# Kernel optimization log

Measured on AMD Instinct MI355X. Metric: run time of the kernel, lower is better.

The kernel has to match this reference:

```python
import jax, jax.numpy as jnp
import numpy as np

N_NODES = 10000
N_EDGES = 320000
IN_DIM, HID_DIM, OUT_DIM = 256, 512, 256


def gcn_conv(x, src, dst, W, b, n_nodes):
    """PyG GCNConv: add self-loops, symmetric deg normalization, linear, scatter-add, bias."""
    loops = jnp.arange(n_nodes, dtype=src.dtype)
    s = jnp.concatenate([src, loops])
    d = jnp.concatenate([dst, loops])
    deg = jax.ops.segment_sum(jnp.ones_like(s, dtype=x.dtype), d, num_segments=n_nodes)
    dinv = jax.lax.rsqrt(deg)  # deg >= 1 due to self-loops
    norm = dinv[s] * dinv[d]  # [E+N]
    h = x @ W  # [N, out]
    msg = h[s] * norm[:, None]  # [E+N, out]
    return jax.ops.segment_sum(msg, d, num_segments=n_nodes) + b


def setup_inputs() -> dict:
    key = jax.random.key(0)
    ks = jax.random.split(key, 8)
    x = jax.random.normal(ks[0], (N_NODES, IN_DIM), dtype=jnp.float32)
    edge_index = jax.random.randint(ks[1], (2, N_EDGES), 0, N_NODES, dtype=jnp.int64 if jax.config.jax_enable_x64 else jnp.int32)
    perturb_first = jax.random.normal(ks[2], (N_NODES, HID_DIM), dtype=jnp.float32)
    perturb_last = jax.random.normal(ks[3], (N_NODES, OUT_DIM), dtype=jnp.float32)
    W1 = jax.random.normal(ks[4], (IN_DIM, HID_DIM), dtype=jnp.float32) * (1.0 / np.sqrt(IN_DIM))
    b1 = jnp.zeros((HID_DIM,), dtype=jnp.float32)
    W2 = jax.random.normal(ks[5], (HID_DIM, OUT_DIM), dtype=jnp.float32) * (1.0 / np.sqrt(HID_DIM))
    b2 = jnp.zeros((OUT_DIM,), dtype=jnp.float32)
    return {"x": x, "edge_index": edge_index, "perturb_first": perturb_first,
            "perturb_last": perturb_last, "W1": W1, "b1": b1, "W2": W2, "b2": b2}


def reference(x, edge_index, perturb_first, perturb_last, W1, b1, W2, b2):
    # Faithful to Encoder_Adversarial_GCN.forward: only model[0] (conv1) and
    # model[3] (conv2) are applied; LayerNorm/PReLU layers are skipped.
    src, dst = edge_index[0], edge_index[1]
    h = gcn_conv(x, src, dst, W1, b1, N_NODES) + perturb_first
    out = gcn_conv(h, src, dst, W2, b2, N_NODES) + perturb_last
    return out
```

## Files before the change

### kernel.cpp

```cpp
#include <hip/hip_runtime.h>
#include <hip/hip_bf16.h>

#define NN 10000
#define NE 320000
#define IN_DIM 256
#define HID_DIM 512
#define OUT_DIM 256
#define CAP 96

typedef __attribute__((ext_vector_type(8))) short sh8;
typedef __attribute__((ext_vector_type(4))) float f32x4;

__device__ __forceinline__ ushort f2b(float f) {
    uint u = __builtin_bit_cast(uint, f);
    u = (u + 0x7FFFu + ((u >> 16) & 1u)) >> 16;
    return (ushort)u;
}
__device__ __forceinline__ float b2f(ushort h) {
    uint u = ((uint)h) << 16;
    return __builtin_bit_cast(float, u);
}

__device__ __forceinline__ void g2l16(const ushort* g, ushort* l) {
    __builtin_amdgcn_global_load_lds(
        (const __attribute__((address_space(1))) void*)g,
        (__attribute__((address_space(3))) void*)l,
        16, 0, 0);
}

__global__ void k_conv(const float* __restrict__ x, ushort* __restrict__ xb,
                       const float* __restrict__ W1, ushort* __restrict__ W1t,
                       const float* __restrict__ W2, ushort* __restrict__ W2t,
                       int* __restrict__ cursor) {
    const int b = blockIdx.x, t = threadIdx.x;
    if (b < 2500) {
        size_t i = ((size_t)b * 256 + t) * 4;
        float4 f = *(const float4*)&x[i];
        *(ushort4*)&xb[i] = make_ushort4(f2b(f.x), f2b(f.y), f2b(f.z), f2b(f.w));
    } else if (b < 3012) {
        int idx = (b - 2500) * 256 + t;
        int n = idx >> 8, k = idx & 255;
        W1t[idx] = f2b(W1[(size_t)k * HID_DIM + n]);
    } else if (b < 3524) {
        int idx = (b - 3012) * 256 + t;
        int n = idx >> 9, k = idx & 511;
        W2t[idx] = f2b(W2[(size_t)k * OUT_DIM + n]);
    } else {
        int idx = (b - 3524) * 256 + t;
        cursor[idx] = 0;
    }
}

__global__ void k_fill(const int* __restrict__ src, const int* __restrict__ dst,
                       int* cursor, int* __restrict__ edges, int e) {
    int i = blockIdx.x * blockDim.x + threadIdx.x;
    if (i < e) {
        int d = dst[i];
        int pos = atomicAdd(&cursor[d], 1);
        if (pos < CAP) edges[(size_t)d * CAP + pos] = src[i];
    }
}

template <bool FINAL>
__global__ __launch_bounds__(256) void k_agg(const ushort* __restrict__ tbl,
                                             const int* __restrict__ cnt,
                                             const int* __restrict__ edges,
                                             const float* __restrict__ bias,
                                             const float* __restrict__ pert,
                                             void* __restrict__ outv) {
    const int t = threadIdx.x;
    const int b = blockIdx.x;
    const int g = b & 7;
    const int dimhalf = g >> 2;
    const int nodeblk = (b >> 3) * 4 + (g & 3);
    const int v = nodeblk * 4 + (t >> 6);
    const int lane = t & 63;
    const int qtr = lane >> 4;
    const int d0 = dimhalf * 128 + (lane & 15) * 8;
    const int deg = min(cnt[v], CAP);
    const float dv = rsqrtf((float)(deg + 1));
    const int base = (deg * qtr) >> 2;
    const int n = ((deg * (qtr + 1)) >> 2) - base;
    const int* ep = edges + (size_t)v * CAP + base;

    float a[8];
    if (qtr == 0) {
        sh8 hv = *(const sh8*)&tbl[(size_t)v * 256 + d0];
#pragma unroll
        for (int j = 0; j < 8; ++j) a[j] = b2f((ushort)hv[j]) * dv;
    } else {
#pragma unroll
        for (int j = 0; j < 8; ++j) a[j] = 0.f;
    }

    int i = 0;
    for (; i + 2 <= n; i += 2) {
        int s0 = ep[i], s1 = ep[i + 1];
        float w0 = rsqrtf((float)(cnt[s0] + 1));
        float w1 = rsqrtf((float)(cnt[s1] + 1));
        sh8 r0 = *(const sh8*)&tbl[(size_t)s0 * 256 + d0];
        sh8 r1 = *(const sh8*)&tbl[(size_t)s1 * 256 + d0];
#pragma unroll
        for (int j = 0; j < 8; ++j) a[j] = fmaf(b2f((ushort)r0[j]), w0, a[j]);
#pragma unroll
        for (int j = 0; j < 8; ++j) a[j] = fmaf(b2f((ushort)r1[j]), w1, a[j]);
    }
    if (i < n) {
        int s0 = ep[i];
        float w0 = rsqrtf((float)(cnt[s0] + 1));
        sh8 r0 = *(const sh8*)&tbl[(size_t)s0 * 256 + d0];
#pragma unroll
        for (int j = 0; j < 8; ++j) a[j] = fmaf(b2f((ushort)r0[j]), w0, a[j]);
    }

#pragma unroll
    for (int j = 0; j < 8; ++j) {
        a[j] += __shfl_xor(a[j], 16);
        a[j] += __shfl_xor(a[j], 32);
        a[j] *= dv;
    }

    if (qtr == 0) {
        const size_t o = (size_t)v * 256 + d0;
        if (FINAL) {
            float* out = (float*)outv;
            float4 p0 = *(const float4*)&pert[o];
            float4 p1 = *(const float4*)&pert[o + 4];
            float4 b0 = *(const float4*)&bias[d0];
            float4 b1 = *(const float4*)&bias[d0 + 4];
            *(float4*)&out[o]     = make_float4(a[0] + b0.x + p0.x, a[1] + b0.y + p0.y,
                                                a[2] + b0.z + p0.z, a[3] + b0.w + p0.w);
            *(float4*)&out[o + 4] = make_float4(a[4] + b1.x + p1.x, a[5] + b1.y + p1.y,
                                                a[6] + b1.z + p1.z, a[7] + b1.w + p1.w);
        } else {
            ushort* out = (ushort*)outv;
            *(ushort4*)&out[o]     = make_ushort4(f2b(a[0]), f2b(a[1]), f2b(a[2]), f2b(a[3]));
            *(ushort4*)&out[o + 4] = make_ushort4(f2b(a[4]), f2b(a[5]), f2b(a[6]), f2b(a[7]));
        }
    }
}

template <bool BIAS>
__global__ __launch_bounds__(256) void k_gemm(const ushort* __restrict__ A,
                                              const ushort* __restrict__ Bt,
                                              const float* __restrict__ bias,
                                              const float* __restrict__ pert,
                                              ushort* __restrict__ C,
                                              int M, int N, int K) {
    __shared__ ushort As[64][64];
    __shared__ ushort Bs[64][64];
    const int T = gridDim.x;
    const int q = T >> 3, r = T & 7;
    const int xcd = blockIdx.x & 7, jj = blockIdx.x >> 3;
    const int tid = (xcd < r ? xcd * (q + 1) : r * (q + 1) + (xcd - r) * q) + jj;
    const int nbx = N >> 6;
    const int bm = (tid / nbx) * 64;
    const int bn = (tid % nbx) * 64;

    const int t = threadIdx.x;
    const int lane = t & 63;
    const int w = t >> 6;
    const int wm = (w >> 1) * 32, wn = (w & 1) * 32;
    const int fr = lane & 15, kb = lane >> 4;

    const int rho  = lane >> 3;
    const int scol = ((lane & 7) ^ rho) * 8;
    const int c0 = w, c1 = w + 4;
    ushort* lA0 = &As[0][0] + c0 * 512;
    ushort* lA1 = &As[0][0] + c1 * 512;
    ushort* lB0 = &Bs[0][0] + c0 * 512;
    ushort* lB1 = &Bs[0][0] + c1 * 512;
    const ushort* gA0 = A  + (size_t)(bm + c0 * 8 + rho) * K + scol;
    const ushort* gA1 = A  + (size_t)(bm + c1 * 8 + rho) * K + scol;
    const ushort* gB0 = Bt + (size_t)(bn + c0 * 8 + rho) * K + scol;
    const ushort* gB1 = Bt + (size_t)(bn + c1 * 8 + rho) * K + scol;

    f32x4 acc[2][2] = {};

    for (int k0 = 0; k0 < K; k0 += 64) {
        __syncthreads();
        g2l16(gA0, lA0); g2l16(gA1, lA1);
        g2l16(gB0, lB0); g2l16(gB1, lB1);
        gA0 += 64; gA1 += 64; gB0 += 64; gB1 += 64;
        __syncthreads();
#pragma unroll
        for (int ks = 0; ks < 2; ++ks) {
            const int slot = ((ks * 4 + kb) ^ (fr & 7)) * 8;
            sh8 a0 = *(const sh8*)&As[wm + fr][slot];
            sh8 a1 = *(const sh8*)&As[wm + 16 + fr][slot];
            sh8 b0 = *(const sh8*)&Bs[wn + fr][slot];
            sh8 b1 = *(const sh8*)&Bs[wn + 16 + fr][slot];
            acc[0][0] = __builtin_amdgcn_mfma_f32_16x16x32_bf16(a0, b0, acc[0][0], 0, 0, 0);
            acc[0][1] = __builtin_amdgcn_mfma_f32_16x16x32_bf16(a0, b1, acc[0][1], 0, 0, 0);
            acc[1][0] = __builtin_amdgcn_mfma_f32_16x16x32_bf16(a1, b0, acc[1][0], 0, 0, 0);
            acc[1][1] = __builtin_amdgcn_mfma_f32_16x16x32_bf16(a1, b1, acc[1][1], 0, 0, 0);
        }
    }

#pragma unroll
    for (int fm = 0; fm < 2; ++fm)
#pragma unroll
        for (int i = 0; i < 4; ++i) {
            int row = bm + wm + fm * 16 + (lane >> 4) * 4 + i;
            if (row < M) {
#pragma unroll
                for (int fn = 0; fn < 2; ++fn) {
                    int col = bn + wn + fn * 16 + fr;
                    float val = acc[fm][fn][i];
                    if (BIAS) val += bias[col] + pert[(size_t)row * N + col];
                    C[(size_t)row * N + col] = f2b(val);
                }
            }
        }
}

extern "C" void kernel_launch(void* const* d_in, const int* in_sizes, int n_in,
                              void* d_out, int out_size, void* d_ws, size_t ws_size,
                              hipStream_t stream) {
    const float* x  = (const float*)d_in[0];
    const int*   ei = (const int*)d_in[1];
    const float* pf = (const float*)d_in[2];
    const float* pl = (const float*)d_in[3];
    const float* W1 = (const float*)d_in[4];
    const float* b1 = (const float*)d_in[5];
    const float* W2 = (const float*)d_in[6];
    const float* b2 = (const float*)d_in[7];
    float* out = (float*)d_out;

    const int* src = ei;
    const int* dst = ei + NE;

    char* p = (char*)d_ws;
    int*    cursor = (int*)p;            p += 10240 * 4;
    int*    edges  = (int*)p;            p += (size_t)NN * CAP * 4;
    ushort* xb     = (ushort*)p;         p += (size_t)NN * IN_DIM * 2;
    ushort* xa     = (ushort*)p;         p += (size_t)NN * IN_DIM * 2;
    ushort* W1t    = (ushort*)p;         p += (size_t)IN_DIM * HID_DIM * 2;
    ushort* W2t    = (ushort*)p;         p += (size_t)HID_DIM * OUT_DIM * 2;
    ushort* hmid   = (ushort*)p;         p += (size_t)NN * HID_DIM * 2;
    ushort* h2     = (ushort*)p;         p += (size_t)NN * OUT_DIM * 2;

    k_conv<<<3564, 256, 0, stream>>>(x, xb, W1, W1t, W2, W2t, cursor);
    k_fill<<<(NE + 255) / 256, 256, 0, stream>>>(src, dst, cursor, edges, NE);

    const int nby = (NN + 63) / 64;

    k_agg<false><<<(NN / 4) * 2, 256, 0, stream>>>(xb, cursor, edges, nullptr, nullptr, xa);
    k_gemm<true><<<(HID_DIM / 64) * nby, 256, 0, stream>>>(
        xa, W1t, b1, pf, hmid, NN, HID_DIM, IN_DIM);

    k_gemm<false><<<(OUT_DIM / 64) * nby, 256, 0, stream>>>(
        hmid, W2t, nullptr, nullptr, h2, NN, OUT_DIM, HID_DIM);
    k_agg<true><<<(NN / 4) * 2, 256, 0, stream>>>(h2, cursor, edges, b2, pl, (void*)out);
}
```

Before: 89.23 us.

## Double-buffer GEMM LDS tiles with compile-time K and nontemporal agg accesses

The GEMM now takes K as a template parameter and double-buffers the A/B LDS tiles. It prefetches the next k-tile via global_load_lds before computing the current one, with explicit vmcnt waits and barriers. The aggregation kernel switches edge-index loads, perturbation loads and output stores to nontemporal hints. The goal is to hide global-to-LDS latency in the GEMMs and to reduce cache pollution from streaming data, at the cost of doubled LDS use and hand-managed wait counts.

Result: slower. 104.3 us (median of 2 runs) (+16.9%).

```diff
diff --git a/kernel.cpp b/kernel.cpp
--- a/kernel.cpp
+++ b/kernel.cpp
@@ -10,6 +10,7 @@
 
 typedef __attribute__((ext_vector_type(8))) short sh8;
 typedef __attribute__((ext_vector_type(4))) float f32x4;
+typedef __attribute__((ext_vector_type(4))) ushort u16x4;
 
 __device__ __forceinline__ ushort f2b(float f) {
     uint u = __builtin_bit_cast(uint, f);
@@ -95,7 +96,8 @@
 
     int i = 0;
     for (; i + 2 <= n; i += 2) {
-        int s0 = ep[i], s1 = ep[i + 1];
+        int s0 = __builtin_nontemporal_load(ep + i);
+        int s1 = __builtin_nontemporal_load(ep + i + 1);
         float w0 = rsqrtf((float)(cnt[s0] + 1));
         float w1 = rsqrtf((float)(cnt[s1] + 1));
         sh8 r0 = *(const sh8*)&tbl[(size_t)s0 * 256 + d0];
@@ -106,7 +108,7 @@
         for (int j = 0; j < 8; ++j) a[j] = fmaf(b2f((ushort)r1[j]), w1, a[j]);
     }
     if (i < n) {
-        int s0 = ep[i];
+        int s0 = __builtin_nontemporal_load(ep + i);
         float w0 = rsqrtf((float)(cnt[s0] + 1));
         sh8 r0 = *(const sh8*)&tbl[(size_t)s0 * 256 + d0];
 #pragma unroll
@@ -124,31 +126,35 @@
         const size_t o = (size_t)v * 256 + d0;
         if (FINAL) {
             float* out = (float*)outv;
-            float4 p0 = *(const float4*)&pert[o];
-            float4 p1 = *(const float4*)&pert[o + 4];
-            float4 b0 = *(const float4*)&bias[d0];
-            float4 b1 = *(const float4*)&bias[d0 + 4];
-            *(float4*)&out[o]     = make_float4(a[0] + b0.x + p0.x, a[1] + b0.y + p0.y,
-                                                a[2] + b0.z + p0.z, a[3] + b0.w + p0.w);
-            *(float4*)&out[o + 4] = make_float4(a[4] + b1.x + p1.x, a[5] + b1.y + p1.y,
-                                                a[6] + b1.z + p1.z, a[7] + b1.w + p1.w);
+            f32x4 p0 = __builtin_nontemporal_load((const f32x4*)&pert[o]);
+            f32x4 p1 = __builtin_nontemporal_load((const f32x4*)&pert[o + 4]);
+            const float4 b0 = *(const float4*)&bias[d0];
+            const float4 b1 = *(const float4*)&bias[d0 + 4];
+            f32x4 o0 = {a[0] + b0.x + p0.x, a[1] + b0.y + p0.y,
+                        a[2] + b0.z + p0.z, a[3] + b0.w + p0.w};
+            f32x4 o1 = {a[4] + b1.x + p1.x, a[5] + b1.y + p1.y,
+                        a[6] + b1.z + p1.z, a[7] + b1.w + p1.w};
+            __builtin_nontemporal_store(o0, (f32x4*)&out[o]);
+            __builtin_nontemporal_store(o1, (f32x4*)&out[o + 4]);
         } else {
             ushort* out = (ushort*)outv;
-            *(ushort4*)&out[o]     = make_ushort4(f2b(a[0]), f2b(a[1]), f2b(a[2]), f2b(a[3]));
-            *(ushort4*)&out[o + 4] = make_ushort4(f2b(a[4]), f2b(a[5]), f2b(a[6]), f2b(a[7]));
-        }
-    }
-}
-
-template <bool BIAS>
+            u16x4 o0 = {f2b(a[0]), f2b(a[1]), f2b(a[2]), f2b(a[3])};
+            u16x4 o1 = {f2b(a[4]), f2b(a[5]), f2b(a[6]), f2b(a[7])};
+            __builtin_nontemporal_store(o0, (u16x4*)&out[o]);
+            __builtin_nontemporal_store(o1, (u16x4*)&out[o + 4]);
+        }
+    }
+}
+
+template <bool BIAS, int K>
 __global__ __launch_bounds__(256) void k_gemm(const ushort* __restrict__ A,
                                               const ushort* __restrict__ Bt,
                                               const float* __restrict__ bias,
                                               const float* __restrict__ pert,
                                               ushort* __restrict__ C,
-                                              int M, int N, int K) {
-    __shared__ ushort As[64][64];
-    __shared__ ushort Bs[64][64];
+                                              int M, int N) {
+    __shared__ ushort As[2][64][64];
+    __shared__ ushort Bs[2][64][64];
     const int T = gridDim.x;
     const int q = T >> 3, r = T & 7;
     const int xcd = blockIdx.x & 7, jj = blockIdx.x >> 3;
@@ -166,35 +172,46 @@
     const int rho  = lane >> 3;
     const int scol = ((lane & 7) ^ rho) * 8;
     const int c0 = w, c1 = w + 4;
-    ushort* lA0 = &As[0][0] + c0 * 512;
-    ushort* lA1 = &As[0][0] + c1 * 512;
-    ushort* lB0 = &Bs[0][0] + c0 * 512;
-    ushort* lB1 = &Bs[0][0] + c1 * 512;
     const ushort* gA0 = A  + (size_t)(bm + c0 * 8 + rho) * K + scol;
     const ushort* gA1 = A  + (size_t)(bm + c1 * 8 + rho) * K + scol;
     const ushort* gB0 = Bt + (size_t)(bn + c0 * 8 + rho) * K + scol;
     const ushort* gB1 = Bt + (size_t)(bn + c1 * 8 + rho) * K + scol;
 
     f32x4 acc[2][2] = {};
-
-    for (int k0 = 0; k0 < K; k0 += 64) {
-        __syncthreads();
-        g2l16(gA0, lA0); g2l16(gA1, lA1);
-        g2l16(gB0, lB0); g2l16(gB1, lB1);
-        gA0 += 64; gA1 += 64; gB0 += 64; gB1 += 64;
-        __syncthreads();
+    constexpr int NT = K >> 6;
+
+    g2l16(gA0, &As[0][0][0] + c0 * 512); g2l16(gA1, &As[0][0][0] + c1 * 512);
+    g2l16(gB0, &Bs[0][0][0] + c0 * 512); g2l16(gB1, &Bs[0][0][0] + c1 * 512);
+    gA0 += 64; gA1 += 64; gB0 += 64; gB1 += 64;
+
+#pragma unroll
+    for (int kt = 0; kt < NT; ++kt) {
+        const int sel = kt & 1;
+        if (kt + 1 < NT) {
+            const int sx = sel ^ 1;
+            g2l16(gA0, &As[sx][0][0] + c0 * 512); g2l16(gA1, &As[sx][0][0] + c1 * 512);
+            g2l16(gB0, &Bs[sx][0][0] + c0 * 512); g2l16(gB1, &Bs[sx][0][0] + c1 * 512);
+            gA0 += 64; gA1 += 64; gB0 += 64; gB1 += 64;
+            asm volatile("s_waitcnt vmcnt(4)" ::: "memory");
+        } else {
+            asm volatile("s_waitcnt vmcnt(0)" ::: "memory");
+        }
+        __builtin_amdgcn_s_barrier();
+        __builtin_amdgcn_sched_barrier(0);
 #pragma unroll
         for (int ks = 0; ks < 2; ++ks) {
             const int slot = ((ks * 4 + kb) ^ (fr & 7)) * 8;
-            sh8 a0 = *(const sh8*)&As[wm + fr][slot];
-            sh8 a1 = *(const sh8*)&As[wm + 16 + fr][slot];
-            sh8 b0 = *(const sh8*)&Bs[wn + fr][slot];
-            sh8 b1 = *(const sh8*)&Bs[wn + 16 + fr][slot];
+            sh8 a0 = *(const sh8*)&As[sel][wm + fr][slot];
+            sh8 a1 = *(const sh8*)&As[sel][wm + 16 + fr][slot];
+            sh8 b0 = *(const sh8*)&Bs[sel][wn + fr][slot];
+            sh8 b1 = *(const sh8*)&Bs[sel][wn + 16 + fr][slot];
             acc[0][0] = __builtin_amdgcn_mfma_f32_16x16x32_bf16(a0, b0, acc[0][0], 0, 0, 0);
             acc[0][1] = __builtin_amdgcn_mfma_f32_16x16x32_bf16(a0, b1, acc[0][1], 0, 0, 0);
             acc[1][0] = __builtin_amdgcn_mfma_f32_16x16x32_bf16(a1, b0, acc[1][0], 0, 0, 0);
             acc[1][1] = __builtin_amdgcn_mfma_f32_16x16x32_bf16(a1, b1, acc[1][1], 0, 0, 0);
         }
+        __builtin_amdgcn_sched_barrier(0);
+        __builtin_amdgcn_s_barrier();
     }
 
 #pragma unroll
@@ -246,10 +263,10 @@
     const int nby = (NN + 63) / 64;
 
     k_agg<false><<<(NN / 4) * 2, 256, 0, stream>>>(xb, cursor, edges, nullptr, nullptr, xa);
-    k_gemm<true><<<(HID_DIM / 64) * nby, 256, 0, stream>>>(
-        xa, W1t, b1, pf, hmid, NN, HID_DIM, IN_DIM);
-
-    k_gemm<false><<<(OUT_DIM / 64) * nby, 256, 0, stream>>>(
-        hmid, W2t, nullptr, nullptr, h2, NN, OUT_DIM, HID_DIM);
+    k_gemm<true, IN_DIM><<<(HID_DIM / 64) * nby, 256, 0, stream>>>(
+        xa, W1t, b1, pf, hmid, NN, HID_DIM);
+
+    k_gemm<false, HID_DIM><<<(OUT_DIM / 64) * nby, 256, 0, stream>>>(
+        hmid, W2t, nullptr, nullptr, h2, NN, OUT_DIM);
     k_agg<true><<<(NN / 4) * 2, 256, 0, stream>>>(h2, cursor, edges, b2, pl, (void*)out);
 }
```
